# Optimization experiments

Hardware: AMD Instinct MI355X
Metric: run time of the kernel (lower is better)

The kernel has to match this reference:

```python
import jax, jax.numpy as jnp
import numpy as np

N_II = 100000      # item nodes
N_UIU = 200000     # user + item nodes
D = 64             # embedding_dim
E_II = 600000
E_UIU = 1200000
L_II = 3           # num_layers_ii
L_UIU = 3          # num_layers_uiu
N_USERS = 100000   # items occupy indices [N_USERS, N_USERS+N_II)


def _lightgcn_embedding(x, edge_index, edge_weight, num_layers, num_nodes):
    """PyG LightGCN.get_embedding: symmetric gcn_norm (no self loops) + mean over layer outputs."""
    src, dst = edge_index[0], edge_index[1]
    # gcn_norm: deg over target nodes, weighted by edge_weight
    deg = jax.ops.segment_sum(edge_weight, dst, num_segments=num_nodes)
    deg_inv_sqrt = jnp.where(deg > 0, jax.lax.rsqrt(jnp.where(deg > 0, deg, 1.0)), 0.0)
    norm = deg_inv_sqrt[src] * edge_weight * deg_inv_sqrt[dst]  # [E]
    alpha = 1.0 / (num_layers + 1)
    out = x * alpha
    for _ in range(num_layers):
        # SpMM: gather source embeddings, scale, scatter-add to targets
        x = jax.ops.segment_sum(norm[:, None] * x[src], dst, num_segments=num_nodes)  # [N, D]
        out = out + x * alpha
    return out


def setup_inputs() -> dict:
    key = jax.random.key(0)
    k1, k2, k3, k4, k5, k6 = jax.random.split(key, 6)
    return {
        "emb_ii": jax.random.normal(k1, (N_II, D), dtype=jnp.float32),
        "emb_uiu": jax.random.normal(k2, (N_UIU, D), dtype=jnp.float32),
        "edge_attr_ii": jax.random.uniform(k3, (E_II,), dtype=jnp.float32),
        "edge_attr_uiu": jax.random.uniform(k4, (E_UIU,), dtype=jnp.float32),
        "edge_index_ii": jax.random.randint(k5, (2, E_II), 0, N_II, dtype=jnp.int32),
        "edge_index_uiu": jax.random.randint(k6, (2, E_UIU), 0, N_UIU, dtype=jnp.int32),
        # contiguous item block starting at N_USERS (node_mask_item.nonzero())
        "item_idx": jnp.arange(N_II, dtype=jnp.int32) + N_USERS,
    }


def reference(emb_ii, emb_uiu, edge_attr_ii, edge_attr_uiu,
              edge_index_ii, edge_index_uiu, item_idx):
    # item-item graph propagation
    h_ii = _lightgcn_embedding(emb_ii, edge_index_ii, edge_attr_ii, L_II, N_II)  # [N_II, D]
    # write item embeddings into the user-item embedding table
    emb_uiu = emb_uiu.at[item_idx].set(h_ii)
    # user-item graph propagation
    h_uiu = _lightgcn_embedding(emb_uiu, edge_index_uiu, edge_attr_uiu, L_UIU, N_UIU)  # [N_UIU, D]
    return h_uiu
```

## Files before the change

### kernel.cpp

```cpp
#include <hip/hip_runtime.h>


#define D       64
#define N_II    100000
#define N_UIU   200000
#define E_II    600000
#define E_UIU   1200000
#define N_USERS 100000

__device__ __forceinline__ unsigned short f2bf(float f) {
    unsigned u = __float_as_uint(f);
    u += 0x7fffu + ((u >> 16) & 1u);
    return (unsigned short)(u >> 16);
}
__device__ __forceinline__ void bf8_fma(float acc[8], uint4 p, float v) {
    acc[0] += v * __uint_as_float(p.x << 16);
    acc[1] += v * __uint_as_float(p.x & 0xffff0000u);
    acc[2] += v * __uint_as_float(p.y << 16);
    acc[3] += v * __uint_as_float(p.y & 0xffff0000u);
    acc[4] += v * __uint_as_float(p.z << 16);
    acc[5] += v * __uint_as_float(p.z & 0xffff0000u);
    acc[6] += v * __uint_as_float(p.w << 16);
    acc[7] += v * __uint_as_float(p.w & 0xffff0000u);
}
__device__ __forceinline__ void bf8_add(float acc[8], uint4 p) {
    acc[0] += __uint_as_float(p.x << 16);
    acc[1] += __uint_as_float(p.x & 0xffff0000u);
    acc[2] += __uint_as_float(p.y << 16);
    acc[3] += __uint_as_float(p.y & 0xffff0000u);
    acc[4] += __uint_as_float(p.z << 16);
    acc[5] += __uint_as_float(p.z & 0xffff0000u);
    acc[6] += __uint_as_float(p.w << 16);
    acc[7] += __uint_as_float(p.w & 0xffff0000u);
}
__device__ __forceinline__ uint4 pack8(const float a[8]) {
    uint4 r;
    r.x = (unsigned)f2bf(a[0]) | ((unsigned)f2bf(a[1]) << 16);
    r.y = (unsigned)f2bf(a[2]) | ((unsigned)f2bf(a[3]) << 16);
    r.z = (unsigned)f2bf(a[4]) | ((unsigned)f2bf(a[5]) << 16);
    r.w = (unsigned)f2bf(a[6]) | ((unsigned)f2bf(a[7]) << 16);
    return r;
}


#define CR_K 8
__global__ void k_cnt_rank(const int* __restrict__ dst, int* __restrict__ cnt,
                           int* __restrict__ rank, int E) {
    int base = blockIdx.x * (blockDim.x * CR_K) + threadIdx.x;
    int d[CR_K];
#pragma unroll
    for (int k = 0; k < CR_K; ++k) {
        int e = base + k * blockDim.x;
        d[k] = (e < E) ? dst[e] : 0;
    }
#pragma unroll
    for (int k = 0; k < CR_K; ++k) {
        int e = base + k * blockDim.x;
        if (e < E) rank[e] = atomicAdd(&cnt[d[k]], 1);
    }
}

__global__ void k_rowoff(const int* __restrict__ cnt, int2* __restrict__ rr,
                         int* __restrict__ gcur, int N) {
    __shared__ int sh[256];
    __shared__ int base;
    int t = threadIdx.x;
    int i = blockIdx.x * 256 + t;
    int v = (i < N) ? cnt[i] : 0;
    sh[t] = v;
    __syncthreads();
    for (int off = 1; off < 256; off <<= 1) {
        int u = (t >= off) ? sh[t - off] : 0;
        __syncthreads();
        sh[t] += u;
        __syncthreads();
    }
    if (t == 255) base = atomicAdd(gcur, sh[255]);
    __syncthreads();
    if (i < N) {
        int o = base + sh[t] - v;
        rr[i] = make_int2(o, o + v);
    }
}

#define FE_K 4
__global__ void k_fillE(const int* __restrict__ src, const int* __restrict__ dst,
                        const float* __restrict__ w, const int* __restrict__ rank,
                        const int2* __restrict__ rr, int2* __restrict__ ev, int E) {
    int base = blockIdx.x * (blockDim.x * FE_K) + threadIdx.x;
    int d[FE_K], r[FE_K], s[FE_K];
    float ww[FE_K];
#pragma unroll
    for (int k = 0; k < FE_K; ++k) {
        int e = base + k * blockDim.x;
        if (e < E) { d[k] = dst[e]; r[k] = rank[e]; s[k] = src[e]; ww[k] = w[e]; }
        else       { d[k] = 0; r[k] = 0; s[k] = 0; ww[k] = 0.f; }
    }
    int pos[FE_K];
#pragma unroll
    for (int k = 0; k < FE_K; ++k) pos[k] = rr[d[k]].x + r[k];
#pragma unroll
    for (int k = 0; k < FE_K; ++k) {
        int e = base + k * blockDim.x;
        if (e < E) ev[pos[k]] = make_int2(s[k], __float_as_int(ww[k]));
    }
}

__global__ void k_deg_hist(const int2* __restrict__ rr, const int2* __restrict__ ev,
                           float* __restrict__ dis, int* __restrict__ binrank,
                           int* __restrict__ ghist, int N) {
    __shared__ int h[64];
    __shared__ int hbase[64];
    int t = threadIdx.x;
    if (t < 64) h[t] = 0;
    __syncthreads();
    int i = blockIdx.x * 256 + t;
    int b = 0, rk = 0;
    if (i < N) {
        int2 se = rr[i];
        float dg = 0.f;
        for (int j = se.x; j < se.y; ++j) dg += __int_as_float(ev[j].y);
        dis[i] = (dg > 0.f) ? rsqrtf(dg) : 0.f;
        int c = se.y - se.x;
        b = (c < 63) ? c : 63;
        rk = atomicAdd(&h[b], 1);
    }
    __syncthreads();
    if (t < 64) hbase[t] = h[t] ? atomicAdd(&ghist[t], h[t]) : 0;
    __syncthreads();
    if (i < N) binrank[i] = hbase[b] + rk;
}

__global__ void k_scan64(const int* __restrict__ ghist, int* __restrict__ gboff) {
    int l = threadIdx.x;
    int v = ghist[l];
    int s = v;
    for (int o = 1; o < 64; o <<= 1) {
        int u = __shfl_up(s, o);
        if (l >= o) s += u;
    }
    gboff[l] = s - v;
}

__global__ void k_val_scatter(const int2* __restrict__ rr, const float* __restrict__ dis,
                              const int* __restrict__ binrank, const int* __restrict__ gboff,
                              int2* __restrict__ ev, int* __restrict__ perm,
                              int2* __restrict__ rrp, int N) {
    int i = blockIdx.x * blockDim.x + threadIdx.x;
    if (i >= N) return;
    int2 se = rr[i];
    float di = dis[i];
    for (int j = se.x; j < se.y; ++j) {
        int2 p = ev[j];
        ev[j].y = __float_as_int(di * __int_as_float(p.y) * dis[p.x]);
    }
    int c = se.y - se.x;
    int b = (c < 63) ? c : 63;
    int pos = gboff[b] + binrank[i];
    perm[pos] = i;
    rrp[pos]  = rr[i];
}

__global__ void k_cvt(const float4* __restrict__ x, uint4* __restrict__ xb, int n8) {
    int i = blockIdx.x * blockDim.x + threadIdx.x;
    if (i >= n8) return;
    float4 a = x[2 * i], b = x[2 * i + 1];
    float t[8] = {a.x, a.y, a.z, a.w, b.x, b.y, b.z, b.w};
    xb[i] = pack8(t);
}

__global__ void k_spmm8(const int2* __restrict__ rrp, const int* __restrict__ perm,
                        const int2* __restrict__ ev, const uint4* __restrict__ xb,
                        uint4* __restrict__ xn, int N) {
    int idx = blockIdx.x * blockDim.x + threadIdx.x;
    int vrow = idx >> 3;
    if (vrow >= N) return;
    int g = idx & 7;
    int2 se = rrp[vrow];
    int row = perm[vrow];
    float acc[8] = {0.f, 0.f, 0.f, 0.f, 0.f, 0.f, 0.f, 0.f};
    int j = se.x, e = se.y;
    for (; j + 3 < e; j += 4) {
        int2 p0 = ev[j], p1 = ev[j + 1], p2 = ev[j + 2], p3 = ev[j + 3];
        uint4 a0 = xb[p0.x * 8 + g];
        uint4 a1 = xb[p1.x * 8 + g];
        uint4 a2 = xb[p2.x * 8 + g];
        uint4 a3 = xb[p3.x * 8 + g];
        bf8_fma(acc, a0, __int_as_float(p0.y));
        bf8_fma(acc, a1, __int_as_float(p1.y));
        bf8_fma(acc, a2, __int_as_float(p2.y));
        bf8_fma(acc, a3, __int_as_float(p3.y));
    }
    for (; j < e; ++j) {
        int2 p0 = ev[j];
        uint4 a0 = xb[p0.x * 8 + g];
        bf8_fma(acc, a0, __int_as_float(p0.y));
    }
    xn[row * 8 + g] = pack8(acc);
}

__global__ void k_spmm8_final(const int2* __restrict__ rrp, const int* __restrict__ perm,
                              const int2* __restrict__ ev, const uint4* __restrict__ x2b,
                              const uint4* __restrict__ x1b, const uint4* __restrict__ x0b,
                              float4* __restrict__ out, uint4* __restrict__ outb,
                              float alpha, int N) {
    int idx = blockIdx.x * blockDim.x + threadIdx.x;
    int vrow = idx >> 3;
    if (vrow >= N) return;
    int g = idx & 7;
    int2 se = rrp[vrow];
    int row = perm[vrow];
    float acc[8] = {0.f, 0.f, 0.f, 0.f, 0.f, 0.f, 0.f, 0.f};
    int j = se.x, e = se.y;
    for (; j + 3 < e; j += 4) {
        int2 p0 = ev[j], p1 = ev[j + 1], p2 = ev[j + 2], p3 = ev[j + 3];
        uint4 a0 = x2b[p0.x * 8 + g];
        uint4 a1 = x2b[p1.x * 8 + g];
        uint4 a2 = x2b[p2.x * 8 + g];
        uint4 a3 = x2b[p3.x * 8 + g];
        bf8_fma(acc, a0, __int_as_float(p0.y));
        bf8_fma(acc, a1, __int_as_float(p1.y));
        bf8_fma(acc, a2, __int_as_float(p2.y));
        bf8_fma(acc, a3, __int_as_float(p3.y));
    }
    for (; j < e; ++j) {
        int2 p0 = ev[j];
        uint4 a0 = x2b[p0.x * 8 + g];
        bf8_fma(acc, a0, __int_as_float(p0.y));
    }
    bf8_add(acc, x1b[row * 8 + g]);
    bf8_add(acc, x2b[row * 8 + g]);
    bf8_add(acc, x0b[row * 8 + g]);
    float r[8];
#pragma unroll
    for (int k = 0; k < 8; ++k) r[k] = alpha * acc[k];
    if (out) {
        out[row * 16 + 2 * g]     = make_float4(r[0], r[1], r[2], r[3]);
        out[row * 16 + 2 * g + 1] = make_float4(r[4], r[5], r[6], r[7]);
    }
    if (outb) outb[row * 8 + g] = pack8(r);
}


static void build_csr(const int* src, const int* dst, const float* w, int E, int N,
                      int2* ev, int* rank, int* cnt, int2* rr, float* dis,
                      int* perm, int2* rrp, hipStream_t stream) {
    const int B = 256;
    const int nbN = (N + B - 1) / B;
    const int nbE_cr = (E + B * CR_K - 1) / (B * CR_K);
    const int nbE_fe = (E + B * FE_K - 1) / (B * FE_K);
    int* gcur  = cnt + N;
    int* ghist = cnt + N + 1;
    int* gboff = cnt + N + 65;
    int* binrank = rank;
    hipMemsetAsync(cnt, 0, ((size_t)N + 65) * sizeof(int), stream);
    k_cnt_rank   <<<nbE_cr, B, 0, stream>>>(dst, cnt, rank, E);
    k_rowoff     <<<nbN, B, 0, stream>>>(cnt, rr, gcur, N);
    k_fillE      <<<nbE_fe, B, 0, stream>>>(src, dst, w, rank, rr, ev, E);
    k_deg_hist   <<<nbN, B, 0, stream>>>(rr, ev, dis, binrank, ghist, N);
    k_scan64     <<<1, 64, 0, stream>>>(ghist, gboff);
    k_val_scatter<<<nbN, B, 0, stream>>>(rr, dis, binrank, gboff, ev, perm, rrp, N);
}

extern "C" void kernel_launch(void* const* d_in, const int* in_sizes, int n_in,
                              void* d_out, int out_size, void* d_ws, size_t ws_size,
                              hipStream_t stream) {
    const float* emb_ii  = (const float*)d_in[0];
    const float* emb_uiu = (const float*)d_in[1];
    const float* w_ii    = (const float*)d_in[2];
    const float* w_uiu   = (const float*)d_in[3];
    const int*   src_ii  = (const int*)d_in[4];
    const int*   dst_ii  = src_ii + E_II;
    const int*   src_uiu = (const int*)d_in[5];
    const int*   dst_uiu = src_uiu + E_UIU;
    float*       out     = (float*)d_out;

    uint4* xb0_u = (uint4*)d_ws;
    uint4* x1_u  = xb0_u + (size_t)N_UIU * 8;
    uint4* x2_u  = x1_u + (size_t)N_UIU * 8;
    int2*  ev    = (int2*)(x2_u + (size_t)N_UIU * 8);
    int*   rank  = (int*)(ev + E_UIU);
    int2*  rr    = (int2*)(rank + E_UIU);
    int*   cnt   = (int*)(rr + N_UIU);
    float* dis   = (float*)(cnt + N_UIU + 129);

    uint4* g1_x0 = x1_u;
    uint4* g1_x1 = x1_u + (size_t)N_II * 8;
    uint4* g1_x2 = x2_u;

    const int B = 256;
    const float alpha = 0.25f;

    {
        int*  perm = rank + N_II;
        int2* rrp  = (int2*)(rank + 2 * N_II);
        build_csr(src_ii, dst_ii, w_ii, E_II, N_II, ev, rank, cnt, rr, dis,
                  perm, rrp, stream);
        const int n8 = N_II * 8;
        const int ng = (n8 + B - 1) / B;
        uint4* hii_b = xb0_u + (size_t)N_USERS * 8;
        k_cvt  <<<ng, B, 0, stream>>>((const float4*)emb_ii, g1_x0, n8);
        k_spmm8<<<ng, B, 0, stream>>>(rrp, perm, ev, g1_x0, g1_x1, N_II);
        k_spmm8<<<ng, B, 0, stream>>>(rrp, perm, ev, g1_x1, g1_x2, N_II);
        k_spmm8_final<<<ng, B, 0, stream>>>(rrp, perm, ev, g1_x2, g1_x1, g1_x0,
                                            nullptr, hii_b, alpha, N_II);
    }

    {
        int*  perm = rank + N_UIU;
        int2* rrp  = (int2*)(rank + 2 * N_UIU);
        build_csr(src_uiu, dst_uiu, w_uiu, E_UIU, N_UIU, ev, rank, cnt, rr, dis,
                  perm, rrp, stream);
        const int n8u = N_USERS * 8;
        k_cvt<<<(n8u + B - 1) / B, B, 0, stream>>>((const float4*)emb_uiu, xb0_u, n8u);
        const int n8 = N_UIU * 8;
        const int ng = (n8 + B - 1) / B;
        k_spmm8<<<ng, B, 0, stream>>>(rrp, perm, ev, xb0_u, x1_u, N_UIU);
        k_spmm8<<<ng, B, 0, stream>>>(rrp, perm, ev, x1_u, x2_u, N_UIU);
        k_spmm8_final<<<ng, B, 0, stream>>>(rrp, perm, ev, x2_u, x1_u, xb0_u,
                                            (float4*)out, nullptr, alpha, N_UIU);
    }
}
```

Before: 498.5 us.

## Use per-XCC private counters and fuse degree and normalization into CSR build

Edge counting now keeps a private count and weighted-degree array per XCC, selected by the hardware XCC id. It uses workgroup-scope relaxed atomics to reduce contention on shared counters, and accumulates degree in the same pass. A node kernel merges the eight per-XCC partials into row offsets, inverse square-root degrees, per-XCC base offsets and the degree histogram. The fill kernel then writes already-normalized edge values, which removes the separate pass that re-read every edge to sum degrees and rescale weights. In exchange it adds a memset of eight-times-larger count/degree buffers, placed in the spare half of a workspace buffer, and its correctness depends on workgroup-scope atomics being coherent across CUs within one XCC.

```diff
diff --git a/kernel.cpp b/kernel.cpp
--- a/kernel.cpp
+++ b/kernel.cpp
@@ -44,31 +44,65 @@
 
 
 #define CR_K 8
-__global__ void k_cnt_rank(const int* __restrict__ dst, int* __restrict__ cnt,
-                           int* __restrict__ rank, int E) {
+__global__ void k_cnt_rank(const int* __restrict__ dst, const float* __restrict__ w,
+                           int* __restrict__ cntx, float* __restrict__ degx,
+                           int* __restrict__ rank, int E, int N) {
+    int xcc;
+    asm volatile("s_getreg_b32 %0, hwreg(HW_REG_XCC_ID)" : "=s"(xcc));
+    xcc &= 7;
+    int*   cnt = cntx + (size_t)xcc * N;
+    float* deg = degx + (size_t)xcc * N;
     int base = blockIdx.x * (blockDim.x * CR_K) + threadIdx.x;
-    int d[CR_K];
+    int d[CR_K]; float ww[CR_K];
 #pragma unroll
     for (int k = 0; k < CR_K; ++k) {
         int e = base + k * blockDim.x;
-        d[k] = (e < E) ? dst[e] : 0;
+        d[k]  = (e < E) ? dst[e] : 0;
+        ww[k] = (e < E) ? w[e] : 0.f;
     }
 #pragma unroll
     for (int k = 0; k < CR_K; ++k) {
         int e = base + k * blockDim.x;
-        if (e < E) rank[e] = atomicAdd(&cnt[d[k]], 1);
-    }
-}
-
-__global__ void k_rowoff(const int* __restrict__ cnt, int2* __restrict__ rr,
-                         int* __restrict__ gcur, int N) {
+        if (e < E) {
+            int r = __hip_atomic_fetch_add(&cnt[d[k]], 1,
+                                           __ATOMIC_RELAXED, __HIP_MEMORY_SCOPE_WORKGROUP);
+            __hip_atomic_fetch_add(&deg[d[k]], ww[k],
+                                   __ATOMIC_RELAXED, __HIP_MEMORY_SCOPE_WORKGROUP);
+            rank[e] = (xcc << 26) | r;
+        }
+    }
+}
+
+__global__ void k_node(int* __restrict__ cntx, const float* __restrict__ degx,
+                       int2* __restrict__ rr, float* __restrict__ dis,
+                       int* __restrict__ binrank, int* __restrict__ ghist,
+                       int* __restrict__ gcur, int N) {
     __shared__ int sh[256];
+    __shared__ int h[64], hb[64];
     __shared__ int base;
     int t = threadIdx.x;
     int i = blockIdx.x * 256 + t;
-    int v = (i < N) ? cnt[i] : 0;
-    sh[t] = v;
+    int px[8];
+    int c = 0;
+    if (i < N) {
+        int s = 0;
+#pragma unroll
+        for (int x = 0; x < 8; ++x) {
+            int v = cntx[(size_t)x * N + i];
+            px[x] = s; s += v;
+        }
+        c = s;
+        float dg = 0.f;
+#pragma unroll
+        for (int x = 0; x < 8; ++x) dg += degx[(size_t)x * N + i];
+        dis[i] = (dg > 0.f) ? rsqrtf(dg) : 0.f;
+    }
+    int b = (c < 63) ? c : 63;
+    sh[t] = c;
+    if (t < 64) h[t] = 0;
     __syncthreads();
+    int rk = 0;
+    if (i < N) rk = atomicAdd(&h[b], 1);
     for (int off = 1; off < 256; off <<= 1) {
         int u = (t >= off) ? sh[t - off] : 0;
         __syncthreads();
@@ -76,59 +110,15 @@
         __syncthreads();
     }
     if (t == 255) base = atomicAdd(gcur, sh[255]);
+    if (t < 64) hb[t] = h[t] ? atomicAdd(&ghist[t], h[t]) : 0;
     __syncthreads();
     if (i < N) {
-        int o = base + sh[t] - v;
-        rr[i] = make_int2(o, o + v);
-    }
-}
-
-#define FE_K 4
-__global__ void k_fillE(const int* __restrict__ src, const int* __restrict__ dst,
-                        const float* __restrict__ w, const int* __restrict__ rank,
-                        const int2* __restrict__ rr, int2* __restrict__ ev, int E) {
-    int base = blockIdx.x * (blockDim.x * FE_K) + threadIdx.x;
-    int d[FE_K], r[FE_K], s[FE_K];
-    float ww[FE_K];
-#pragma unroll
-    for (int k = 0; k < FE_K; ++k) {
-        int e = base + k * blockDim.x;
-        if (e < E) { d[k] = dst[e]; r[k] = rank[e]; s[k] = src[e]; ww[k] = w[e]; }
-        else       { d[k] = 0; r[k] = 0; s[k] = 0; ww[k] = 0.f; }
-    }
-    int pos[FE_K];
-#pragma unroll
-    for (int k = 0; k < FE_K; ++k) pos[k] = rr[d[k]].x + r[k];
-#pragma unroll
-    for (int k = 0; k < FE_K; ++k) {
-        int e = base + k * blockDim.x;
-        if (e < E) ev[pos[k]] = make_int2(s[k], __float_as_int(ww[k]));
-    }
-}
-
-__global__ void k_deg_hist(const int2* __restrict__ rr, const int2* __restrict__ ev,
-                           float* __restrict__ dis, int* __restrict__ binrank,
-                           int* __restrict__ ghist, int N) {
-    __shared__ int h[64];
-    __shared__ int hbase[64];
-    int t = threadIdx.x;
-    if (t < 64) h[t] = 0;
-    __syncthreads();
-    int i = blockIdx.x * 256 + t;
-    int b = 0, rk = 0;
-    if (i < N) {
-        int2 se = rr[i];
-        float dg = 0.f;
-        for (int j = se.x; j < se.y; ++j) dg += __int_as_float(ev[j].y);
-        dis[i] = (dg > 0.f) ? rsqrtf(dg) : 0.f;
-        int c = se.y - se.x;
-        b = (c < 63) ? c : 63;
-        rk = atomicAdd(&h[b], 1);
-    }
-    __syncthreads();
-    if (t < 64) hbase[t] = h[t] ? atomicAdd(&ghist[t], h[t]) : 0;
-    __syncthreads();
-    if (i < N) binrank[i] = hbase[b] + rk;
+        int o = base + sh[t] - c;
+        rr[i] = make_int2(o, o + c);
+        binrank[i] = hb[b] + rk;
+#pragma unroll
+        for (int x = 0; x < 8; ++x) cntx[(size_t)x * N + i] = o + px[x];
+    }
 }
 
 __global__ void k_scan64(const int* __restrict__ ghist, int* __restrict__ gboff) {
@@ -142,23 +132,44 @@
     gboff[l] = s - v;
 }
 
-__global__ void k_val_scatter(const int2* __restrict__ rr, const float* __restrict__ dis,
-                              const int* __restrict__ binrank, const int* __restrict__ gboff,
-                              int2* __restrict__ ev, int* __restrict__ perm,
-                              int2* __restrict__ rrp, int N) {
+#define FE_K 4
+__global__ void k_fillE(const int* __restrict__ src, const int* __restrict__ dst,
+                        const float* __restrict__ w, const int* __restrict__ rank,
+                        const int* __restrict__ cntx ,
+                        const float* __restrict__ dis,
+                        int2* __restrict__ ev, int E, int N) {
+    int base = blockIdx.x * (blockDim.x * FE_K) + threadIdx.x;
+    int d[FE_K], r[FE_K], s[FE_K]; float ww[FE_K];
+#pragma unroll
+    for (int k = 0; k < FE_K; ++k) {
+        int e = base + k * blockDim.x;
+        if (e < E) { d[k] = dst[e]; r[k] = rank[e]; s[k] = src[e]; ww[k] = w[e]; }
+        else       { d[k] = 0; r[k] = 0; s[k] = 0; ww[k] = 0.f; }
+    }
+    int pos[FE_K]; float val[FE_K];
+#pragma unroll
+    for (int k = 0; k < FE_K; ++k) {
+        pos[k] = cntx[(size_t)(r[k] >> 26) * N + d[k]] + (r[k] & 0x03ffffffu);
+        val[k] = dis[d[k]] * ww[k] * dis[s[k]];
+    }
+#pragma unroll
+    for (int k = 0; k < FE_K; ++k) {
+        int e = base + k * blockDim.x;
+        if (e < E) ev[pos[k]] = make_int2(s[k], __float_as_int(val[k]));
+    }
+}
+
+__global__ void k_scatter(const int2* __restrict__ rr, const int* __restrict__ binrank,
+                          const int* __restrict__ gboff,
+                          int* __restrict__ perm, int2* __restrict__ rrp, int N) {
     int i = blockIdx.x * blockDim.x + threadIdx.x;
     if (i >= N) return;
     int2 se = rr[i];
-    float di = dis[i];
-    for (int j = se.x; j < se.y; ++j) {
-        int2 p = ev[j];
-        ev[j].y = __float_as_int(di * __int_as_float(p.y) * dis[p.x]);
-    }
     int c = se.y - se.x;
     int b = (c < 63) ? c : 63;
     int pos = gboff[b] + binrank[i];
     perm[pos] = i;
-    rrp[pos]  = rr[i];
+    rrp[pos]  = se;
 }
 
 __global__ void k_cvt(const float4* __restrict__ x, uint4* __restrict__ xb, int n8) {
@@ -243,23 +254,23 @@
 
 
 static void build_csr(const int* src, const int* dst, const float* w, int E, int N,
-                      int2* ev, int* rank, int* cnt, int2* rr, float* dis,
-                      int* perm, int2* rrp, hipStream_t stream) {
+                      int2* ev, int* rank, int* cntx, float* degx, int2* rr,
+                      float* dis, int* gtail ,
+                      int* binrank, int* perm, int2* rrp, hipStream_t stream) {
     const int B = 256;
     const int nbN = (N + B - 1) / B;
     const int nbE_cr = (E + B * CR_K - 1) / (B * CR_K);
     const int nbE_fe = (E + B * FE_K - 1) / (B * FE_K);
-    int* gcur  = cnt + N;
-    int* ghist = cnt + N + 1;
-    int* gboff = cnt + N + 65;
-    int* binrank = rank;
-    hipMemsetAsync(cnt, 0, ((size_t)N + 65) * sizeof(int), stream);
-    k_cnt_rank   <<<nbE_cr, B, 0, stream>>>(dst, cnt, rank, E);
-    k_rowoff     <<<nbN, B, 0, stream>>>(cnt, rr, gcur, N);
-    k_fillE      <<<nbE_fe, B, 0, stream>>>(src, dst, w, rank, rr, ev, E);
-    k_deg_hist   <<<nbN, B, 0, stream>>>(rr, ev, dis, binrank, ghist, N);
-    k_scan64     <<<1, 64, 0, stream>>>(ghist, gboff);
-    k_val_scatter<<<nbN, B, 0, stream>>>(rr, dis, binrank, gboff, ev, perm, rrp, N);
+    int* gcur  = gtail;
+    int* ghist = gtail + 1;
+    int* gboff = gtail + 65;
+    hipMemsetAsync(cntx, 0, (size_t)16 * N * sizeof(int), stream);
+    hipMemsetAsync(gtail, 0, 65 * sizeof(int), stream);
+    k_cnt_rank<<<nbE_cr, B, 0, stream>>>(dst, w, cntx, degx, rank, E, N);
+    k_node    <<<nbN, B, 0, stream>>>(cntx, degx, rr, dis, binrank, ghist, gcur, N);
+    k_scan64  <<<1, 64, 0, stream>>>(ghist, gboff);
+    k_fillE   <<<nbE_fe, B, 0, stream>>>(src, dst, w, rank, cntx, dis, ev, E, N);
+    k_scatter <<<nbN, B, 0, stream>>>(rr, binrank, gboff, perm, rrp, N);
 }
 
 extern "C" void kernel_launch(void* const* d_in, const int* in_sizes, int n_in,
@@ -281,8 +292,12 @@
     int2*  ev    = (int2*)(x2_u + (size_t)N_UIU * 8);
     int*   rank  = (int*)(ev + E_UIU);
     int2*  rr    = (int2*)(rank + E_UIU);
-    int*   cnt   = (int*)(rr + N_UIU);
-    float* dis   = (float*)(cnt + N_UIU + 129);
+    int*   gtail = (int*)(rr + N_UIU);
+    float* dis   = (float*)(gtail + 129);
+    int*   binrank = (int*)(dis + N_UIU);
+
+    int*   cntx  = (int*)(x2_u + (size_t)N_UIU * 4);
+    float* degx  = (float*)(cntx + (size_t)8 * N_UIU);
 
     uint4* g1_x0 = x1_u;
     uint4* g1_x1 = x1_u + (size_t)N_II * 8;
@@ -292,10 +307,12 @@
     const float alpha = 0.25f;
 
     {
+        int*   cx = cntx;
+        float* dx = (float*)(cntx + (size_t)8 * N_II);
         int*  perm = rank + N_II;
         int2* rrp  = (int2*)(rank + 2 * N_II);
-        build_csr(src_ii, dst_ii, w_ii, E_II, N_II, ev, rank, cnt, rr, dis,
-                  perm, rrp, stream);
+        build_csr(src_ii, dst_ii, w_ii, E_II, N_II, ev, rank, cx, dx, rr, dis,
+                  gtail, binrank, perm, rrp, stream);
         const int n8 = N_II * 8;
         const int ng = (n8 + B - 1) / B;
         uint4* hii_b = xb0_u + (size_t)N_USERS * 8;
@@ -307,10 +324,12 @@
     }
 
     {
+        int*   cx = cntx;
+        float* dx = (float*)(cntx + (size_t)8 * N_UIU);
         int*  perm = rank + N_UIU;
         int2* rrp  = (int2*)(rank + 2 * N_UIU);
-        build_csr(src_uiu, dst_uiu, w_uiu, E_UIU, N_UIU, ev, rank, cnt, rr, dis,
-                  perm, rrp, stream);
+        build_csr(src_uiu, dst_uiu, w_uiu, E_UIU, N_UIU, ev, rank, cx, dx, rr, dis,
+                  gtail, binrank, perm, rrp, stream);
         const int n8u = N_USERS * 8;
         k_cvt<<<(n8u + B - 1) / B, B, 0, stream>>>((const float4*)emb_uiu, xb0_u, n8u);
         const int n8 = N_UIU * 8;
```

After: 596.6 us. 19.7% more time.

## Overlap second-graph CSR build with first-graph stages via fused multi-role kernels

Applied to the files above, without the earlier changes.

Gives the two graphs separate workspace so the user-item edge counting can be split into chunks. Each chunk runs as extra blocks inside the item-item build and SpMM kernels, and the user-item row-offset pass is fused into the item-item final SpMM. The degree histogram moves into the row-offset pass, and the 64-bin scan is folded into the value-scatter kernel, which removes several launches. This fills the GPU during the small item-item stages, at the cost of more workspace and heterogeneous blocks that may compete for cache and atomics.

```diff
diff --git a/kernel.cpp b/kernel.cpp
--- a/kernel.cpp
+++ b/kernel.cpp
@@ -7,6 +7,9 @@
 #define E_II    600000
 #define E_UIU   1200000
 #define N_USERS 100000
+#define B       256
+#define CR_K    8
+#define FE_K    4
 
 __device__ __forceinline__ unsigned short f2bf(float f) {
     unsigned u = __float_as_uint(f);
@@ -43,56 +46,75 @@
 }
 
 
-#define CR_K 8
-__global__ void k_cnt_rank(const int* __restrict__ dst, int* __restrict__ cnt,
-                           int* __restrict__ rank, int E) {
-    int base = blockIdx.x * (blockDim.x * CR_K) + threadIdx.x;
+__device__ __forceinline__ void rol_cnt(int bid, const int* __restrict__ dst,
+                                        int* __restrict__ cnt, int* __restrict__ rank,
+                                        int e0, int e1) {
+    int base = e0 + bid * (B * CR_K) + threadIdx.x;
     int d[CR_K];
 #pragma unroll
     for (int k = 0; k < CR_K; ++k) {
-        int e = base + k * blockDim.x;
-        d[k] = (e < E) ? dst[e] : 0;
+        int e = base + k * B;
+        d[k] = (e < e1) ? dst[e] : 0;
     }
 #pragma unroll
     for (int k = 0; k < CR_K; ++k) {
-        int e = base + k * blockDim.x;
-        if (e < E) rank[e] = atomicAdd(&cnt[d[k]], 1);
-    }
-}
-
-__global__ void k_rowoff(const int* __restrict__ cnt, int2* __restrict__ rr,
+        int e = base + k * B;
+        if (e < e1) rank[e] = atomicAdd(&cnt[d[k]], 1);
+    }
+}
+
+__device__ __forceinline__ void rol_cvt(int bid, const float4* __restrict__ x,
+                                        uint4* __restrict__ xb, int n8) {
+    int i = bid * B + threadIdx.x;
+    if (i >= n8) return;
+    float4 a = x[2 * i], b = x[2 * i + 1];
+    float t[8] = {a.x, a.y, a.z, a.w, b.x, b.y, b.z, b.w};
+    xb[i] = pack8(t);
+}
+
+__device__ void rol_node(int bid, const int* __restrict__ cnt, int2* __restrict__ rr,
+                         int* __restrict__ binrank, int* __restrict__ ghist,
                          int* __restrict__ gcur, int N) {
-    __shared__ int sh[256];
-    __shared__ int base;
+    __shared__ int sh[B];
+    __shared__ int h[64], hb[64];
+    __shared__ int sbase;
     int t = threadIdx.x;
-    int i = blockIdx.x * 256 + t;
-    int v = (i < N) ? cnt[i] : 0;
-    sh[t] = v;
+    int i = bid * B + t;
+    int c = (i < N) ? cnt[i] : 0;
+    int b = (c < 63) ? c : 63;
+    sh[t] = c;
+    if (t < 64) h[t] = 0;
     __syncthreads();
-    for (int off = 1; off < 256; off <<= 1) {
+    int rk = 0;
+    if (i < N) rk = atomicAdd(&h[b], 1);
+    for (int off = 1; off < B; off <<= 1) {
         int u = (t >= off) ? sh[t - off] : 0;
         __syncthreads();
         sh[t] += u;
         __syncthreads();
     }
-    if (t == 255) base = atomicAdd(gcur, sh[255]);
+    if (t == B - 1) sbase = atomicAdd(gcur, sh[B - 1]);
+    if (t < 64) hb[t] = h[t] ? atomicAdd(&ghist[t], h[t]) : 0;
     __syncthreads();
     if (i < N) {
-        int o = base + sh[t] - v;
-        rr[i] = make_int2(o, o + v);
-    }
-}
-
-#define FE_K 4
-__global__ void k_fillE(const int* __restrict__ src, const int* __restrict__ dst,
-                        const float* __restrict__ w, const int* __restrict__ rank,
-                        const int2* __restrict__ rr, int2* __restrict__ ev, int E) {
-    int base = blockIdx.x * (blockDim.x * FE_K) + threadIdx.x;
+        int o = sbase + sh[t] - c;
+        rr[i] = make_int2(o, o + c);
+        binrank[i] = hb[b] + rk;
+    }
+}
+
+__device__ __forceinline__ void rol_fillE(int bid, const int* __restrict__ src,
+                                          const int* __restrict__ dst,
+                                          const float* __restrict__ w,
+                                          const int* __restrict__ rank,
+                                          const int2* __restrict__ rr,
+                                          int2* __restrict__ ev, int E) {
+    int base = bid * (B * FE_K) + threadIdx.x;
     int d[FE_K], r[FE_K], s[FE_K];
     float ww[FE_K];
 #pragma unroll
     for (int k = 0; k < FE_K; ++k) {
-        int e = base + k * blockDim.x;
+        int e = base + k * B;
         if (e < E) { d[k] = dst[e]; r[k] = rank[e]; s[k] = src[e]; ww[k] = w[e]; }
         else       { d[k] = 0; r[k] = 0; s[k] = 0; ww[k] = 0.f; }
     }
@@ -101,52 +123,39 @@
     for (int k = 0; k < FE_K; ++k) pos[k] = rr[d[k]].x + r[k];
 #pragma unroll
     for (int k = 0; k < FE_K; ++k) {
-        int e = base + k * blockDim.x;
+        int e = base + k * B;
         if (e < E) ev[pos[k]] = make_int2(s[k], __float_as_int(ww[k]));
     }
 }
 
-__global__ void k_deg_hist(const int2* __restrict__ rr, const int2* __restrict__ ev,
-                           float* __restrict__ dis, int* __restrict__ binrank,
-                           int* __restrict__ ghist, int N) {
-    __shared__ int h[64];
-    __shared__ int hbase[64];
+__device__ __forceinline__ void rol_deg(int bid, const int2* __restrict__ rr,
+                                        const int2* __restrict__ ev,
+                                        float* __restrict__ dis, int N) {
+    int i = bid * B + threadIdx.x;
+    if (i >= N) return;
+    int2 se = rr[i];
+    float dg = 0.f;
+    for (int j = se.x; j < se.y; ++j) dg += __int_as_float(ev[j].y);
+    dis[i] = (dg > 0.f) ? rsqrtf(dg) : 0.f;
+}
+
+__device__ void rol_valsc(int bid, const int2* __restrict__ rr, const float* __restrict__ dis,
+                          const int* __restrict__ binrank, const int* __restrict__ ghist,
+                          int2* __restrict__ ev, int* __restrict__ perm,
+                          int2* __restrict__ rrp, int N) {
+    __shared__ int sboff[64];
     int t = threadIdx.x;
-    if (t < 64) h[t] = 0;
+    if (t < 64) {
+        int v = ghist[t];
+        int s = v;
+        for (int o = 1; o < 64; o <<= 1) {
+            int u = __shfl_up(s, o);
+            if (t >= o) s += u;
+        }
+        sboff[t] = s - v;
+    }
     __syncthreads();
-    int i = blockIdx.x * 256 + t;
-    int b = 0, rk = 0;
-    if (i < N) {
-        int2 se = rr[i];
-        float dg = 0.f;
-        for (int j = se.x; j < se.y; ++j) dg += __int_as_float(ev[j].y);
-        dis[i] = (dg > 0.f) ? rsqrtf(dg) : 0.f;
-        int c = se.y - se.x;
-        b = (c < 63) ? c : 63;
-        rk = atomicAdd(&h[b], 1);
-    }
-    __syncthreads();
-    if (t < 64) hbase[t] = h[t] ? atomicAdd(&ghist[t], h[t]) : 0;
-    __syncthreads();
-    if (i < N) binrank[i] = hbase[b] + rk;
-}
-
-__global__ void k_scan64(const int* __restrict__ ghist, int* __restrict__ gboff) {
-    int l = threadIdx.x;
-    int v = ghist[l];
-    int s = v;
-    for (int o = 1; o < 64; o <<= 1) {
-        int u = __shfl_up(s, o);
-        if (l >= o) s += u;
-    }
-    gboff[l] = s - v;
-}
-
-__global__ void k_val_scatter(const int2* __restrict__ rr, const float* __restrict__ dis,
-                              const int* __restrict__ binrank, const int* __restrict__ gboff,
-                              int2* __restrict__ ev, int* __restrict__ perm,
-                              int2* __restrict__ rrp, int N) {
-    int i = blockIdx.x * blockDim.x + threadIdx.x;
+    int i = bid * B + t;
     if (i >= N) return;
     int2 se = rr[i];
     float di = dis[i];
@@ -156,23 +165,15 @@
     }
     int c = se.y - se.x;
     int b = (c < 63) ? c : 63;
-    int pos = gboff[b] + binrank[i];
+    int pos = sboff[b] + binrank[i];
     perm[pos] = i;
-    rrp[pos]  = rr[i];
-}
-
-__global__ void k_cvt(const float4* __restrict__ x, uint4* __restrict__ xb, int n8) {
-    int i = blockIdx.x * blockDim.x + threadIdx.x;
-    if (i >= n8) return;
-    float4 a = x[2 * i], b = x[2 * i + 1];
-    float t[8] = {a.x, a.y, a.z, a.w, b.x, b.y, b.z, b.w};
-    xb[i] = pack8(t);
-}
-
-__global__ void k_spmm8(const int2* __restrict__ rrp, const int* __restrict__ perm,
-                        const int2* __restrict__ ev, const uint4* __restrict__ xb,
-                        uint4* __restrict__ xn, int N) {
-    int idx = blockIdx.x * blockDim.x + threadIdx.x;
+    rrp[pos]  = se;
+}
+
+__device__ void rol_spmm(int bid, const int2* __restrict__ rrp, const int* __restrict__ perm,
+                         const int2* __restrict__ ev, const uint4* __restrict__ xb,
+                         uint4* __restrict__ xn, int N) {
+    int idx = bid * B + threadIdx.x;
     int vrow = idx >> 3;
     if (vrow >= N) return;
     int g = idx & 7;
@@ -199,12 +200,12 @@
     xn[row * 8 + g] = pack8(acc);
 }
 
-__global__ void k_spmm8_final(const int2* __restrict__ rrp, const int* __restrict__ perm,
-                              const int2* __restrict__ ev, const uint4* __restrict__ x2b,
-                              const uint4* __restrict__ x1b, const uint4* __restrict__ x0b,
-                              float4* __restrict__ out, uint4* __restrict__ outb,
-                              float alpha, int N) {
-    int idx = blockIdx.x * blockDim.x + threadIdx.x;
+__device__ void rol_final(int bid, const int2* __restrict__ rrp, const int* __restrict__ perm,
+                          const int2* __restrict__ ev, const uint4* __restrict__ x2b,
+                          const uint4* __restrict__ x1b, const uint4* __restrict__ x0b,
+                          float4* __restrict__ out, uint4* __restrict__ outb,
+                          float alpha, int N) {
+    int idx = bid * B + threadIdx.x;
     int vrow = idx >> 3;
     if (vrow >= N) return;
     int g = idx & 7;
@@ -242,25 +243,88 @@
 }
 
 
-static void build_csr(const int* src, const int* dst, const float* w, int E, int N,
-                      int2* ev, int* rank, int* cnt, int2* rr, float* dis,
-                      int* perm, int2* rrp, hipStream_t stream) {
-    const int B = 256;
-    const int nbN = (N + B - 1) / B;
-    const int nbE_cr = (E + B * CR_K - 1) / (B * CR_K);
-    const int nbE_fe = (E + B * FE_K - 1) / (B * FE_K);
-    int* gcur  = cnt + N;
-    int* ghist = cnt + N + 1;
-    int* gboff = cnt + N + 65;
-    int* binrank = rank;
-    hipMemsetAsync(cnt, 0, ((size_t)N + 65) * sizeof(int), stream);
-    k_cnt_rank   <<<nbE_cr, B, 0, stream>>>(dst, cnt, rank, E);
-    k_rowoff     <<<nbN, B, 0, stream>>>(cnt, rr, gcur, N);
-    k_fillE      <<<nbE_fe, B, 0, stream>>>(src, dst, w, rank, rr, ev, E);
-    k_deg_hist   <<<nbN, B, 0, stream>>>(rr, ev, dis, binrank, ghist, N);
-    k_scan64     <<<1, 64, 0, stream>>>(ghist, gboff);
-    k_val_scatter<<<nbN, B, 0, stream>>>(rr, dis, binrank, gboff, ev, perm, rrp, N);
-}
+__global__ void f_cnt_cvt2(int nbA, const int* dstA, int* cntA, int* rankA, int eA,
+                           int nbB, const float4* xB, uint4* xbB, int n8B,
+                           const float4* xC, uint4* xbC, int n8C) {
+    int b = (int)blockIdx.x;
+    if (b < nbA)       { rol_cnt(b, dstA, cntA, rankA, 0, eA); return; }
+    b -= nbA;
+    if (b < nbB)       { rol_cvt(b, xB, xbB, n8B); return; }
+    rol_cvt(b - nbB, xC, xbC, n8C);
+}
+
+__global__ void f_node_cnt(int nbA, const int* cntN, int2* rr, int* brk, int* ghist,
+                           int* gcur, int N,
+                           const int* dstS, int* cntS, int* rankS, int e0, int e1) {
+    int b = (int)blockIdx.x;
+    if (b < nbA) rol_node(b, cntN, rr, brk, ghist, gcur, N);
+    else         rol_cnt(b - nbA, dstS, cntS, rankS, e0, e1);
+}
+
+__global__ void f_fillE_cnt(int nbA, const int* src, const int* dst, const float* w,
+                            const int* rank, const int2* rr, int2* ev, int E,
+                            const int* dstS, int* cntS, int* rankS, int e0, int e1) {
+    int b = (int)blockIdx.x;
+    if (b < nbA) rol_fillE(b, src, dst, w, rank, rr, ev, E);
+    else         rol_cnt(b - nbA, dstS, cntS, rankS, e0, e1);
+}
+
+__global__ void f_deg_cnt(int nbA, const int2* rr, const int2* ev, float* dis, int N,
+                          const int* dstS, int* cntS, int* rankS, int e0, int e1) {
+    int b = (int)blockIdx.x;
+    if (b < nbA) rol_deg(b, rr, ev, dis, N);
+    else         rol_cnt(b - nbA, dstS, cntS, rankS, e0, e1);
+}
+
+__global__ void f_valsc_cnt(int nbA, const int2* rr, const float* dis, const int* brk,
+                            const int* ghist, int2* ev, int* perm, int2* rrp, int N,
+                            const int* dstS, int* cntS, int* rankS, int e0, int e1) {
+    int b = (int)blockIdx.x;
+    if (b < nbA) rol_valsc(b, rr, dis, brk, ghist, ev, perm, rrp, N);
+    else         rol_cnt(b - nbA, dstS, cntS, rankS, e0, e1);
+}
+
+__global__ void f_spmm_cnt(int nbA, const int2* rrp, const int* perm, const int2* ev,
+                           const uint4* xb, uint4* xn, int N,
+                           const int* dstS, int* cntS, int* rankS, int e0, int e1) {
+    int b = (int)blockIdx.x;
+    if (b < nbA) rol_spmm(b, rrp, perm, ev, xb, xn, N);
+    else         rol_cnt(b - nbA, dstS, cntS, rankS, e0, e1);
+}
+
+__global__ void f_final_node(int nbA, const int2* rrpA, const int* permA, const int2* evA,
+                             const uint4* x2b, const uint4* x1b, const uint4* x0b,
+                             float4* outA, uint4* outbA, float alpha, int NA,
+                             const int* cntN, int2* rrB, int* brkB, int* ghistB,
+                             int* gcurB, int NB) {
+    int b = (int)blockIdx.x;
+    if (b < nbA) rol_final(b, rrpA, permA, evA, x2b, x1b, x0b, outA, outbA, alpha, NA);
+    else         rol_node(b - nbA, cntN, rrB, brkB, ghistB, gcurB, NB);
+}
+
+__global__ void k_fillE(const int* src, const int* dst, const float* w, const int* rank,
+                        const int2* rr, int2* ev, int E) {
+    rol_fillE((int)blockIdx.x, src, dst, w, rank, rr, ev, E);
+}
+__global__ void k_deg(const int2* rr, const int2* ev, float* dis, int N) {
+    rol_deg((int)blockIdx.x, rr, ev, dis, N);
+}
+__global__ void k_valsc(const int2* rr, const float* dis, const int* brk, const int* ghist,
+                        int2* ev, int* perm, int2* rrp, int N) {
+    rol_valsc((int)blockIdx.x, rr, dis, brk, ghist, ev, perm, rrp, N);
+}
+__global__ void k_spmm8(const int2* rrp, const int* perm, const int2* ev,
+                        const uint4* xb, uint4* xn, int N) {
+    rol_spmm((int)blockIdx.x, rrp, perm, ev, xb, xn, N);
+}
+__global__ void k_spmm8_final(const int2* rrp, const int* perm, const int2* ev,
+                              const uint4* x2b, const uint4* x1b, const uint4* x0b,
+                              float4* out, uint4* outb, float alpha, int N) {
+    rol_final((int)blockIdx.x, rrp, perm, ev, x2b, x1b, x0b, out, outb, alpha, N);
+}
+
+
+static inline int nbx(int work, int per) { return (work + per - 1) / per; }
 
 extern "C" void kernel_launch(void* const* d_in, const int* in_sizes, int n_in,
                               void* d_out, int out_size, void* d_ws, size_t ws_size,
@@ -278,46 +342,87 @@
     uint4* xb0_u = (uint4*)d_ws;
     uint4* x1_u  = xb0_u + (size_t)N_UIU * 8;
     uint4* x2_u  = x1_u + (size_t)N_UIU * 8;
-    int2*  ev    = (int2*)(x2_u + (size_t)N_UIU * 8);
-    int*   rank  = (int*)(ev + E_UIU);
-    int2*  rr    = (int2*)(rank + E_UIU);
-    int*   cnt   = (int*)(rr + N_UIU);
-    float* dis   = (float*)(cnt + N_UIU + 129);
+
+    int2*  ev1   = (int2*)(x2_u + (size_t)N_II * 8);
+    int*   rank1 = (int*)(ev1 + E_II);
+    int2*  rr1   = (int2*)(rank1 + E_II);
+    int*   cnt1  = (int*)(rr1 + N_II);
+    int*   gt1   = cnt1 + N_II;
+    float* dis1  = (float*)(gt1 + 65);
+    int*   brk1  = (int*)(dis1 + N_II);
+    int*   perm1 = rank1;
+    int2*  rrp1  = (int2*)(rank1 + N_II);
+
+    int2*  ev2   = (int2*)(x2_u + (size_t)N_UIU * 8);
+    int*   rank2 = (int*)(ev2 + E_UIU);
+    int2*  rr2   = (int2*)(rank2 + E_UIU);
+    int*   cnt2  = (int*)(rr2 + N_UIU);
+    int*   gt2   = cnt2 + N_UIU;
+    float* dis2  = (float*)(gt2 + 65);
+    int*   brk2  = (int*)(dis2 + N_UIU);
+    int*   perm2 = rank2;
+    int2*  rrp2  = (int2*)(rank2 + N_UIU);
 
     uint4* g1_x0 = x1_u;
     uint4* g1_x1 = x1_u + (size_t)N_II * 8;
     uint4* g1_x2 = x2_u;
-
-    const int B = 256;
+    uint4* hii_b = xb0_u + (size_t)N_USERS * 8;
+
     const float alpha = 0.25f;
 
-    {
-        int*  perm = rank + N_II;
-        int2* rrp  = (int2*)(rank + 2 * N_II);
-        build_csr(src_ii, dst_ii, w_ii, E_II, N_II, ev, rank, cnt, rr, dis,
-                  perm, rrp, stream);
-        const int n8 = N_II * 8;
-        const int ng = (n8 + B - 1) / B;
-        uint4* hii_b = xb0_u + (size_t)N_USERS * 8;
-        k_cvt  <<<ng, B, 0, stream>>>((const float4*)emb_ii, g1_x0, n8);
-        k_spmm8<<<ng, B, 0, stream>>>(rrp, perm, ev, g1_x0, g1_x1, N_II);
-        k_spmm8<<<ng, B, 0, stream>>>(rrp, perm, ev, g1_x1, g1_x2, N_II);
-        k_spmm8_final<<<ng, B, 0, stream>>>(rrp, perm, ev, g1_x2, g1_x1, g1_x0,
-                                            nullptr, hii_b, alpha, N_II);
-    }
-
-    {
-        int*  perm = rank + N_UIU;
-        int2* rrp  = (int2*)(rank + 2 * N_UIU);
-        build_csr(src_uiu, dst_uiu, w_uiu, E_UIU, N_UIU, ev, rank, cnt, rr, dis,
-                  perm, rrp, stream);
-        const int n8u = N_USERS * 8;
-        k_cvt<<<(n8u + B - 1) / B, B, 0, stream>>>((const float4*)emb_uiu, xb0_u, n8u);
-        const int n8 = N_UIU * 8;
-        const int ng = (n8 + B - 1) / B;
-        k_spmm8<<<ng, B, 0, stream>>>(rrp, perm, ev, xb0_u, x1_u, N_UIU);
-        k_spmm8<<<ng, B, 0, stream>>>(rrp, perm, ev, x1_u, x2_u, N_UIU);
-        k_spmm8_final<<<ng, B, 0, stream>>>(rrp, perm, ev, x2_u, x1_u, xb0_u,
-                                            (float4*)out, nullptr, alpha, N_UIU);
-    }
-}
+    hipMemsetAsync(cnt1, 0, ((size_t)N_II + 65) * sizeof(int), stream);
+    hipMemsetAsync(cnt2, 0, ((size_t)N_UIU + 65) * sizeof(int), stream);
+
+    const int s[7] = {0, 128000, 320000, 448000, 640000, 920000, E_UIU};
+
+    const int nbCnt1 = nbx(E_II, B * CR_K);
+    const int nbCvt1 = nbx(N_II * 8, B);
+    const int nbCvt2 = nbx(N_USERS * 8, B);
+    const int nbN1   = nbx(N_II, B);
+    const int nbF1   = nbx(E_II, B * FE_K);
+    const int nbS1   = nbx(N_II * 8, B);
+    const int nbN2   = nbx(N_UIU, B);
+    const int nbF2   = nbx(E_UIU, B * FE_K);
+    const int nbS2   = nbx(N_UIU * 8, B);
+
+    f_cnt_cvt2<<<nbCnt1 + nbCvt1 + nbCvt2, B, 0, stream>>>(
+        nbCnt1, dst_ii, cnt1, rank1, E_II,
+        nbCvt1, (const float4*)emb_ii, g1_x0, N_II * 8,
+        (const float4*)emb_uiu, xb0_u, N_USERS * 8);
+
+    f_node_cnt<<<nbN1 + nbx(s[1] - s[0], B * CR_K), B, 0, stream>>>(
+        nbN1, cnt1, rr1, brk1, gt1 + 1, gt1, N_II,
+        dst_uiu, cnt2, rank2, s[0], s[1]);
+
+    f_fillE_cnt<<<nbF1 + nbx(s[2] - s[1], B * CR_K), B, 0, stream>>>(
+        nbF1, src_ii, dst_ii, w_ii, rank1, rr1, ev1, E_II,
+        dst_uiu, cnt2, rank2, s[1], s[2]);
+
+    f_deg_cnt<<<nbN1 + nbx(s[3] - s[2], B * CR_K), B, 0, stream>>>(
+        nbN1, rr1, ev1, dis1, N_II,
+        dst_uiu, cnt2, rank2, s[2], s[3]);
+
+    f_valsc_cnt<<<nbN1 + nbx(s[4] - s[3], B * CR_K), B, 0, stream>>>(
+        nbN1, rr1, dis1, brk1, gt1 + 1, ev1, perm1, rrp1, N_II,
+        dst_uiu, cnt2, rank2, s[3], s[4]);
+
+    f_spmm_cnt<<<nbS1 + nbx(s[5] - s[4], B * CR_K), B, 0, stream>>>(
+        nbS1, rrp1, perm1, ev1, g1_x0, g1_x1, N_II,
+        dst_uiu, cnt2, rank2, s[4], s[5]);
+
+    f_spmm_cnt<<<nbS1 + nbx(s[6] - s[5], B * CR_K), B, 0, stream>>>(
+        nbS1, rrp1, perm1, ev1, g1_x1, g1_x2, N_II,
+        dst_uiu, cnt2, rank2, s[5], s[6]);
+
+    f_final_node<<<nbS1 + nbN2, B, 0, stream>>>(
+        nbS1, rrp1, perm1, ev1, g1_x2, g1_x1, g1_x0, nullptr, hii_b, alpha, N_II,
+        cnt2, rr2, brk2, gt2 + 1, gt2, N_UIU);
+
+    k_fillE<<<nbF2, B, 0, stream>>>(src_uiu, dst_uiu, w_uiu, rank2, rr2, ev2, E_UIU);
+    k_deg  <<<nbN2, B, 0, stream>>>(rr2, ev2, dis2, N_UIU);
+    k_valsc<<<nbN2, B, 0, stream>>>(rr2, dis2, brk2, gt2 + 1, ev2, perm2, rrp2, N_UIU);
+    k_spmm8<<<nbS2, B, 0, stream>>>(rrp2, perm2, ev2, xb0_u, x1_u, N_UIU);
+    k_spmm8<<<nbS2, B, 0, stream>>>(rrp2, perm2, ev2, x1_u, x2_u, N_UIU);
+    k_spmm8_final<<<nbS2, B, 0, stream>>>(rrp2, perm2, ev2, x2_u, x1_u, xb0_u,
+                                          (float4*)out, nullptr, alpha, N_UIU);
+}
```

After: 480.0 us. 3.7% less time.
